# Kernel tuning notes

Hardware: AMD Instinct MI355X
Metric: run time of the kernel (lower is better)

The kernel has to match this reference:

```python
import jax, jax.numpy as jnp
import numpy as np

D = 768
H = 12
HD = 64
S = 77
FF = 3072
EPS = 1e-5


def _layernorm(x, w, b):
    mu = jnp.mean(x, axis=-1, keepdims=True)
    var = jnp.mean(jnp.square(x - mu), axis=-1, keepdims=True)
    return (x - mu) * jax.lax.rsqrt(var + EPS) * w + b


def setup_inputs() -> dict:
    key = jax.random.key(0)
    ks = jax.random.split(key, 18)
    s = 1.0 / np.sqrt(D)
    sf = 1.0 / np.sqrt(FF)
    return {
        "x": jax.random.normal(ks[0], (512, S, D), dtype=jnp.float32),
        "ln1_w": jnp.ones((D,), jnp.float32),
        "ln1_b": jnp.zeros((D,), jnp.float32),
        "qw": jax.random.uniform(ks[1], (D, D), jnp.float32, -s, s),
        "qb": jax.random.uniform(ks[2], (D,), jnp.float32, -s, s),
        "kw": jax.random.uniform(ks[3], (D, D), jnp.float32, -s, s),
        "kb": jax.random.uniform(ks[4], (D,), jnp.float32, -s, s),
        "vw": jax.random.uniform(ks[5], (D, D), jnp.float32, -s, s),
        "vb": jax.random.uniform(ks[6], (D,), jnp.float32, -s, s),
        "ow": jax.random.uniform(ks[7], (D, D), jnp.float32, -s, s),
        "ob": jax.random.uniform(ks[8], (D,), jnp.float32, -s, s),
        "ln2_w": jnp.ones((D,), jnp.float32),
        "ln2_b": jnp.zeros((D,), jnp.float32),
        "fc1_w": jax.random.uniform(ks[9], (FF, D), jnp.float32, -s, s),
        "fc1_b": jax.random.uniform(ks[10], (FF,), jnp.float32, -s, s),
        "fc2_w": jax.random.uniform(ks[11], (D, FF), jnp.float32, -sf, sf),
        "fc2_b": jax.random.uniform(ks[12], (D,), jnp.float32, -sf, sf),
    }


def reference(x, ln1_w, ln1_b, qw, qb, kw, kb, vw, vb, ow, ob,
              ln2_w, ln2_b, fc1_w, fc1_b, fc2_w, fc2_b):
    B = x.shape[0]
    # --- attention block ---
    h = _layernorm(x, ln1_w, ln1_b)
    q = (h @ qw.T + qb) * 0.125
    k = h @ kw.T + kb
    v = h @ vw.T + vb
    # [B, S, H, HD] -> [B, H, S, HD]
    q = q.reshape(B, S, H, HD).transpose(0, 2, 1, 3)
    k = k.reshape(B, S, H, HD).transpose(0, 2, 1, 3)
    v = v.reshape(B, S, H, HD).transpose(0, 2, 1, 3)
    scores = jnp.einsum('bhqd,bhkd->bhqk', q, k)  # [B,H,S,S]
    # causal additive mask: -inf strictly above diagonal
    mask = jnp.triu(jnp.full((S, S), -jnp.inf, dtype=scores.dtype), 1)
    scores = scores + mask
    attn = jax.nn.softmax(scores, axis=-1)
    ctx = jnp.einsum('bhqk,bhkd->bhqd', attn, v)  # [B,H,S,HD]
    ctx = ctx.transpose(0, 2, 1, 3).reshape(B, S, D)
    x = x + (ctx @ ow.T + ob)
    # --- MLP block with QuickGELU ---
    res = x
    h2 = _layernorm(x, ln2_w, ln2_b) @ fc1_w.T + fc1_b
    h2 = h2 * jax.nn.sigmoid(h2 * 1.702)
    return res + (h2 @ fc2_w.T + fc2_b)
```

## Files before the change

### kernel.cpp

```cpp
#include <hip/hip_runtime.h>

typedef unsigned short u16;
typedef __bf16 v8bf __attribute__((ext_vector_type(8)));
typedef unsigned short u16x8 __attribute__((ext_vector_type(8)));
typedef float v4f __attribute__((ext_vector_type(4)));

#define DEV __device__ __forceinline__

constexpr int M_TOK = 512 * 77;

DEV u16 f2bf(float f) {
  union { float f; unsigned int u; } v; v.f = f;
  unsigned int r = v.u + 0x7fffu + ((v.u >> 16) & 1u);
  return (u16)(r >> 16);
}

DEV void gload16(const void* g, void* l) {
  __builtin_amdgcn_global_load_lds((const __attribute__((address_space(1))) void*)g,
                                   (__attribute__((address_space(3))) void*)l, 16, 0, 0);
}

DEV v4f MF(v8bf a, v8bf b, v4f c) {
  return __builtin_amdgcn_mfma_f32_16x16x32_bf16(a, b, c, 0, 0, 0);
}

__global__ void cvt4_k(const float* __restrict__ src, u16* __restrict__ dst, int n4, float scale) {
  int i = blockIdx.x * blockDim.x + threadIdx.x;
  if (i >= n4) return;
  const float4 v = ((const float4*)src)[i];
  ushort4 o;
  o.x = f2bf(v.x * scale); o.y = f2bf(v.y * scale);
  o.z = f2bf(v.z * scale); o.w = f2bf(v.w * scale);
  ((ushort4*)dst)[i] = o;
}

__global__ void qkvb_k(const float* __restrict__ qb, const float* __restrict__ kb,
                       const float* __restrict__ vb, float* __restrict__ dst) {
  int i = blockIdx.x * 256 + threadIdx.x;
  if (i >= 2304) return;
  dst[i] = (i < 768) ? qb[i] * 0.125f : (i < 1536 ? kb[i - 768] : vb[i - 1536]);
}

__global__ __launch_bounds__(256) void ln_k(const float* __restrict__ x, const float* __restrict__ w,
                                            const float* __restrict__ bvec, u16* __restrict__ out, int nrows) {
  const int lane = threadIdx.x & 63;
  const int row = blockIdx.x * 4 + (threadIdx.x >> 6);
  if (row >= nrows) return;
  const float4* xr = (const float4*)(x + (size_t)row * 768);
  float4 v[3];
  float sum = 0.f, sq = 0.f;
#pragma unroll
  for (int t = 0; t < 3; ++t) {
    v[t] = xr[lane + 64 * t];
    sum += v[t].x + v[t].y + v[t].z + v[t].w;
    sq  += v[t].x * v[t].x + v[t].y * v[t].y + v[t].z * v[t].z + v[t].w * v[t].w;
  }
#pragma unroll
  for (int o = 1; o < 64; o <<= 1) { sum += __shfl_xor(sum, o, 64); sq += __shfl_xor(sq, o, 64); }
  const float mean = sum * (1.f / 768.f);
  const float inv = rsqrtf(sq * (1.f / 768.f) - mean * mean + 1e-5f);
  u16* orow = out + (size_t)row * 768;
#pragma unroll
  for (int t = 0; t < 3; ++t) {
    const int c = 4 * (lane + 64 * t);
    ushort4 o4;
    o4.x = f2bf((v[t].x - mean) * inv * w[c + 0] + bvec[c + 0]);
    o4.y = f2bf((v[t].y - mean) * inv * w[c + 1] + bvec[c + 1]);
    o4.z = f2bf((v[t].z - mean) * inv * w[c + 2] + bvec[c + 2]);
    o4.w = f2bf((v[t].w - mean) * inv * w[c + 3] + bvec[c + 3]);
    *(ushort4*)(orow + c) = o4;
  }
}

template <int OUTF32, int ACT, int RES>
__global__ __launch_bounds__(512, 4) void gemm128_k(
    const u16* __restrict__ A, const u16* __restrict__ Bw,
    const float* __restrict__ bias, const float* __restrict__ res,
    void* __restrict__ out, int M, int N, int K, int nbx) {
  __shared__ u16 lds[32768];
  const int tid = threadIdx.x;
  const int lane = tid & 63;
  const int wv = tid >> 6;
  const int wr = wv >> 2, wc = wv & 3;

  const int nwg = gridDim.x;
  const int q8 = nwg >> 3, r8 = nwg & 7;
  const int xcd = blockIdx.x & 7, cidx = blockIdx.x >> 3;
  const int wg = (xcd < r8 ? xcd * (q8 + 1) : r8 * (q8 + 1) + (xcd - r8) * q8) + cidx;
  const int m0 = (wg / nbx) * 128;
  const int n0 = (wg % nbx) * 128;

  const int frow = lane & 15, fq = lane >> 4;
  const int e = frow & 7;
  const int aB0 = (wr * 64 + frow) * 64 + ((fq ^ e) * 8);
  const int bB0 = 8192 + (wc * 32 + frow) * 64 + ((fq ^ e) * 8);

  const int srow = tid >> 3;
  const int cOff = ((tid & 7) ^ (srow & 7)) * 8;
  const u16* pA = A + (size_t)(m0 + srow) * K + cOff;
  const u16* pB = Bw + (size_t)(n0 + srow) * K + cOff;
  const size_t hk = (size_t)K * 64;
  const int ldsW = wv * 512;

#define LD(IDX) (*(const v8bf*)&lds[IDX])
#define BAR() asm volatile("s_barrier" ::: "memory")
#define VM4() asm volatile("s_waitcnt vmcnt(4)" ::: "memory")
#define VM0() asm volatile("s_waitcnt vmcnt(0)" ::: "memory")
#define STA(kt) do { gload16(pA + (size_t)(kt) * 64, &lds[(((kt) & 1) << 14) + ldsW]); \
                     gload16(pA + hk + (size_t)(kt) * 64, &lds[(((kt) & 1) << 14) + 4096 + ldsW]); } while (0)
#define STB(kt) do { gload16(pB + (size_t)(kt) * 64, &lds[(((kt) & 1) << 14) + 8192 + ldsW]); \
                     gload16(pB + hk + (size_t)(kt) * 64, &lds[(((kt) & 1) << 14) + 12288 + ldsW]); } while (0)

  v4f acc[4][2];
#pragma unroll
  for (int i = 0; i < 4; ++i)
#pragma unroll
    for (int j = 0; j < 2; ++j) acc[i][j] = (v4f){0.f, 0.f, 0.f, 0.f};

  const int NT = K >> 6;

  STA(0); STB(0);
  STA(1); STB(1);
  VM4(); BAR();

#define ITER(kt, STG, VM)                                                       \
  do {                                                                          \
    const int sb = ((kt) & 1) << 14;                                            \
    v8bf a0 = LD(sb + aB0), a1 = LD(sb + aB0 + 1024);                           \
    v8bf a2 = LD(sb + aB0 + 2048), a3 = LD(sb + aB0 + 3072);                    \
    v8bf b0 = LD(sb + bB0), b1 = LD(sb + bB0 + 1024);                           \
    v8bf a4 = LD(sb + (aB0 ^ 32)), a5 = LD(sb + (aB0 ^ 32) + 1024);             \
    v8bf a6 = LD(sb + (aB0 ^ 32) + 2048), a7 = LD(sb + (aB0 ^ 32) + 3072);      \
    v8bf b2 = LD(sb + (bB0 ^ 32)), b3 = LD(sb + (bB0 ^ 32) + 1024);             \
    asm volatile("s_waitcnt lgkmcnt(0)" ::: "memory");                          \
    BAR();             \
    if (STG) { STA((kt) + 2); STB((kt) + 2); }                                  \
    if ((VM) == 4) VM4(); else if ((VM) == 0) VM0();                            \
    __builtin_amdgcn_s_setprio(1);                                              \
    acc[0][0] = MF(a0, b0, acc[0][0]); acc[0][1] = MF(a0, b1, acc[0][1]);       \
    acc[1][0] = MF(a1, b0, acc[1][0]); acc[1][1] = MF(a1, b1, acc[1][1]);       \
    acc[2][0] = MF(a2, b0, acc[2][0]); acc[2][1] = MF(a2, b1, acc[2][1]);       \
    acc[3][0] = MF(a3, b0, acc[3][0]); acc[3][1] = MF(a3, b1, acc[3][1]);       \
    acc[0][0] = MF(a4, b2, acc[0][0]); acc[0][1] = MF(a4, b3, acc[0][1]);       \
    acc[1][0] = MF(a5, b2, acc[1][0]); acc[1][1] = MF(a5, b3, acc[1][1]);       \
    acc[2][0] = MF(a6, b2, acc[2][0]); acc[2][1] = MF(a6, b3, acc[2][1]);       \
    acc[3][0] = MF(a7, b2, acc[3][0]); acc[3][1] = MF(a7, b3, acc[3][1]);       \
    __builtin_amdgcn_s_setprio(0);                                              \
    BAR();              \
  } while (0)

  for (int kt = 0; kt < NT - 2; ++kt) ITER(kt, 1, 4);
  ITER(NT - 2, 0, 0);
  ITER(NT - 1, 0, -1);
#undef ITER
#undef LD
#undef BAR
#undef VM4
#undef VM0
#undef STA
#undef STB

#pragma unroll
  for (int i = 0; i < 4; ++i) {
    const int rowb = m0 + wr * 64 + i * 16 + fq * 4;
#pragma unroll
    for (int j = 0; j < 2; ++j) {
      const int col = n0 + wc * 32 + j * 16 + frow;
      const float bv = bias[col];
#pragma unroll
      for (int rr = 0; rr < 4; ++rr) {
        float v = acc[i][j][rr] + bv;
        if (ACT) v = v * (1.f / (1.f + __expf(-1.702f * v)));
        const size_t off = (size_t)(rowb + rr) * N + col;
        if (RES) v += res[off];
        if (OUTF32) ((float*)out)[off] = v;
        else ((u16*)out)[off] = f2bf(v);
      }
    }
  }
}

__global__ __launch_bounds__(256) void attn_k(const u16* __restrict__ qkv, u16* __restrict__ ctx) {
  __shared__ u16 sQK[10240];
  __shared__ u16 sVt[64 * 120];
  __shared__ float sS[80][81];
  const int tid = threadIdx.x;
  const int lane = tid & 63;
  const int wv = tid >> 6;
  const int b = blockIdx.x / 12;
  const int h = blockIdx.x % 12;
  u16* sQ = sQK;
  u16* sK = sQK + 5120;
  u16* sP = sQK;

  for (int i = tid; i < 10240 + 64 * 120; i += 256) {
    if (i < 10240) sQK[i] = 0; else sVt[i - 10240] = 0;
  }
  __syncthreads();

  const size_t tokBase = (size_t)(b * 77) * 2304 + h * 64;
  for (int c = tid; c < 77 * 8; c += 256) {
    const int row = c >> 3, k8 = (c & 7) * 8;
    const size_t src = tokBase + (size_t)row * 2304 + k8;
    *(u16x8*)&sQ[row * 64 + k8] = *(const u16x8*)&qkv[src];
    *(u16x8*)&sK[row * 64 + k8] = *(const u16x8*)&qkv[src + 768];
    u16x8 v = *(const u16x8*)&qkv[src + 1536];
#pragma unroll
    for (int j = 0; j < 8; ++j) sVt[(k8 + j) * 120 + row] = v[j];
  }
  __syncthreads();

  const int frow = lane & 15, fk = (lane >> 4) * 8;
  for (int t = wv; t < 25; t += 4) {
    const int it = t / 5, jt = t % 5;
    v4f acc = {0.f, 0.f, 0.f, 0.f};
#pragma unroll
    for (int kk = 0; kk < 2; ++kk) {
      v8bf a = *(const v8bf*)&sQ[(it * 16 + frow) * 64 + kk * 32 + fk];
      v8bf bb = *(const v8bf*)&sK[(jt * 16 + frow) * 64 + kk * 32 + fk];
      acc = MF(a, bb, acc);
    }
    const int col = jt * 16 + frow;
#pragma unroll
    for (int r = 0; r < 4; ++r) {
      const int row = it * 16 + (lane >> 4) * 4 + r;
      sS[row][col] = (col > row) ? -1e30f : acc[r];
    }
  }
  __syncthreads();

  if (tid < 80) {
    const int row = tid;
    float mx = -1e30f;
    for (int c2 = 0; c2 < 80; ++c2) mx = fmaxf(mx, sS[row][c2]);
    float sum = 0.f;
    for (int c2 = 0; c2 < 80; ++c2) { float e = __expf(sS[row][c2] - mx); sum += e; sS[row][c2] = e; }
    const float inv = 1.f / sum;
    for (int c2 = 0; c2 < 80; ++c2) sP[row * 96 + c2] = f2bf(sS[row][c2] * inv);
    for (int c2 = 80; c2 < 96; ++c2) sP[row * 96 + c2] = 0;
  }
  __syncthreads();

  const size_t outBase = (size_t)(b * 77) * 768 + h * 64;
  for (int t = wv; t < 20; t += 4) {
    const int it = t / 4, jt = t % 4;
    v4f acc = {0.f, 0.f, 0.f, 0.f};
#pragma unroll
    for (int kk = 0; kk < 3; ++kk) {
      v8bf a = *(const v8bf*)&sP[(it * 16 + frow) * 96 + kk * 32 + fk];
      v8bf bb = *(const v8bf*)&sVt[(jt * 16 + frow) * 120 + kk * 32 + fk];
      acc = MF(a, bb, acc);
    }
    const int col = jt * 16 + frow;
#pragma unroll
    for (int r = 0; r < 4; ++r) {
      const int row = it * 16 + (lane >> 4) * 4 + r;
      if (row < 77) ctx[outBase + (size_t)row * 768 + col] = f2bf(acc[r]);
    }
  }
}

extern "C" void kernel_launch(void* const* d_in, const int* in_sizes, int n_in,
                              void* d_out, int out_size, void* d_ws, size_t ws_size,
                              hipStream_t stream) {
  const float* x    = (const float*)d_in[0];
  const float* ln1w = (const float*)d_in[1];
  const float* ln1b = (const float*)d_in[2];
  const float* qw   = (const float*)d_in[3];
  const float* qb   = (const float*)d_in[4];
  const float* kw   = (const float*)d_in[5];
  const float* kb   = (const float*)d_in[6];
  const float* vw   = (const float*)d_in[7];
  const float* vb   = (const float*)d_in[8];
  const float* ow   = (const float*)d_in[9];
  const float* ob   = (const float*)d_in[10];
  const float* ln2w = (const float*)d_in[11];
  const float* ln2b = (const float*)d_in[12];
  const float* f1wf = (const float*)d_in[13];
  const float* f1b  = (const float*)d_in[14];
  const float* f2wf = (const float*)d_in[15];
  const float* f2b  = (const float*)d_in[16];
  float* outp = (float*)d_out;

  char* p = (char*)d_ws;
  auto alloc = [&](size_t bytes) { char* r = p; p += (bytes + 255) & ~(size_t)255; return r; };
  u16* wqkv = (u16*)alloc((size_t)2304 * 768 * 2);
  u16* owb  = (u16*)alloc((size_t)768 * 768 * 2);
  u16* f1w  = (u16*)alloc((size_t)3072 * 768 * 2);
  u16* f2w  = (u16*)alloc((size_t)768 * 3072 * 2);
  float* qkvb = (float*)alloc(2304 * 4);
  u16* bufA = (u16*)alloc((size_t)M_TOK * 768 * 2);
  u16* bufB = (u16*)alloc((size_t)M_TOK * 3072 * 2);

  cvt4_k<<<576, 256, 0, stream>>>(qw, wqkv, 147456, 0.125f);
  cvt4_k<<<576, 256, 0, stream>>>(kw, wqkv + 589824, 147456, 1.f);
  cvt4_k<<<576, 256, 0, stream>>>(vw, wqkv + 1179648, 147456, 1.f);
  cvt4_k<<<576, 256, 0, stream>>>(ow, owb, 147456, 1.f);
  cvt4_k<<<2304, 256, 0, stream>>>(f1wf, f1w, 589824, 1.f);
  cvt4_k<<<2304, 256, 0, stream>>>(f2wf, f2w, 589824, 1.f);
  qkvb_k<<<9, 256, 0, stream>>>(qb, kb, vb, qkvb);

  ln_k<<<M_TOK / 4, 256, 0, stream>>>(x, ln1w, ln1b, bufA, M_TOK);
  gemm128_k<0, 0, 0><<<308 * 18, 512, 0, stream>>>(bufA, wqkv, qkvb, nullptr, bufB, M_TOK, 2304, 768, 18);
  attn_k<<<512 * 12, 256, 0, stream>>>(bufB, bufA);
  gemm128_k<1, 0, 1><<<308 * 6, 512, 0, stream>>>(bufA, owb, ob, x, outp, M_TOK, 768, 768, 6);
  ln_k<<<M_TOK / 4, 256, 0, stream>>>(outp, ln2w, ln2b, bufA, M_TOK);
  gemm128_k<0, 1, 0><<<308 * 24, 512, 0, stream>>>(bufA, f1w, f1b, nullptr, bufB, M_TOK, 3072, 768, 24);
  gemm128_k<1, 0, 1><<<308 * 6, 512, 0, stream>>>(bufB, f2w, f2b, outp, outp, M_TOK, 768, 3072, 6);
}
```

Before: 952.3 us.

## Use 4-wave GEMM blocks with 64x64 per-wave tiles instead of 8 waves

The 128x128 GEMM tile moves from 8 waves (each 64x32) to 4 waves (each 64x64), with 256 threads per block. Each thread now issues four global-to-LDS loads per operand per k-step, and the wait count rises to match. The goal is more MFMA work per LDS fragment read and fewer waves to synchronise. The cost is twice the accumulator registers per wave and fewer waves available to hide latency.

```diff
diff --git a/kernel.cpp b/kernel.cpp
--- a/kernel.cpp
+++ b/kernel.cpp
@@ -73,7 +73,7 @@
 }
 
 template <int OUTF32, int ACT, int RES>
-__global__ __launch_bounds__(512, 4) void gemm128_k(
+__global__ __launch_bounds__(256, 2) void gemm128_k(
     const u16* __restrict__ A, const u16* __restrict__ Bw,
     const float* __restrict__ bias, const float* __restrict__ res,
     void* __restrict__ out, int M, int N, int K, int nbx) {
@@ -81,7 +81,7 @@
   const int tid = threadIdx.x;
   const int lane = tid & 63;
   const int wv = tid >> 6;
-  const int wr = wv >> 2, wc = wv & 3;
+  const int wr = wv >> 1, wc = wv & 1;
 
   const int nwg = gridDim.x;
   const int q8 = nwg >> 3, r8 = nwg & 7;
@@ -93,69 +93,85 @@
   const int frow = lane & 15, fq = lane >> 4;
   const int e = frow & 7;
   const int aB0 = (wr * 64 + frow) * 64 + ((fq ^ e) * 8);
-  const int bB0 = 8192 + (wc * 32 + frow) * 64 + ((fq ^ e) * 8);
+  const int bB0 = 8192 + (wc * 64 + frow) * 64 + ((fq ^ e) * 8);
 
   const int srow = tid >> 3;
   const int cOff = ((tid & 7) ^ (srow & 7)) * 8;
   const u16* pA = A + (size_t)(m0 + srow) * K + cOff;
   const u16* pB = Bw + (size_t)(n0 + srow) * K + cOff;
-  const size_t hk = (size_t)K * 64;
+  const size_t K32 = (size_t)K * 32;
   const int ldsW = wv * 512;
 
 #define LD(IDX) (*(const v8bf*)&lds[IDX])
 #define BAR() asm volatile("s_barrier" ::: "memory")
-#define VM4() asm volatile("s_waitcnt vmcnt(4)" ::: "memory")
+#define VM8() asm volatile("s_waitcnt vmcnt(8)" ::: "memory")
 #define VM0() asm volatile("s_waitcnt vmcnt(0)" ::: "memory")
-#define STA(kt) do { gload16(pA + (size_t)(kt) * 64, &lds[(((kt) & 1) << 14) + ldsW]); \
-                     gload16(pA + hk + (size_t)(kt) * 64, &lds[(((kt) & 1) << 14) + 4096 + ldsW]); } while (0)
-#define STB(kt) do { gload16(pB + (size_t)(kt) * 64, &lds[(((kt) & 1) << 14) + 8192 + ldsW]); \
-                     gload16(pB + hk + (size_t)(kt) * 64, &lds[(((kt) & 1) << 14) + 12288 + ldsW]); } while (0)
-
-  v4f acc[4][2];
+#define STA(kt) do { const int sb_ = ((kt) & 1) << 14;                              \
+    gload16(pA + 0 * K32 + (size_t)(kt) * 64, &lds[sb_ + 0 * 2048 + ldsW]);         \
+    gload16(pA + 1 * K32 + (size_t)(kt) * 64, &lds[sb_ + 1 * 2048 + ldsW]);         \
+    gload16(pA + 2 * K32 + (size_t)(kt) * 64, &lds[sb_ + 2 * 2048 + ldsW]);         \
+    gload16(pA + 3 * K32 + (size_t)(kt) * 64, &lds[sb_ + 3 * 2048 + ldsW]); } while (0)
+#define STB(kt) do { const int sb_ = (((kt) & 1) << 14) + 8192;                     \
+    gload16(pB + 0 * K32 + (size_t)(kt) * 64, &lds[sb_ + 0 * 2048 + ldsW]);         \
+    gload16(pB + 1 * K32 + (size_t)(kt) * 64, &lds[sb_ + 1 * 2048 + ldsW]);         \
+    gload16(pB + 2 * K32 + (size_t)(kt) * 64, &lds[sb_ + 2 * 2048 + ldsW]);         \
+    gload16(pB + 3 * K32 + (size_t)(kt) * 64, &lds[sb_ + 3 * 2048 + ldsW]); } while (0)
+
+  v4f acc[4][4];
 #pragma unroll
   for (int i = 0; i < 4; ++i)
 #pragma unroll
-    for (int j = 0; j < 2; ++j) acc[i][j] = (v4f){0.f, 0.f, 0.f, 0.f};
+    for (int j = 0; j < 4; ++j) acc[i][j] = (v4f){0.f, 0.f, 0.f, 0.f};
 
   const int NT = K >> 6;
 
   STA(0); STB(0);
   STA(1); STB(1);
-  VM4(); BAR();
+  VM8(); BAR();
 
 #define ITER(kt, STG, VM)                                                       \
   do {                                                                          \
     const int sb = ((kt) & 1) << 14;                                            \
     v8bf a0 = LD(sb + aB0), a1 = LD(sb + aB0 + 1024);                           \
     v8bf a2 = LD(sb + aB0 + 2048), a3 = LD(sb + aB0 + 3072);                    \
-    v8bf b0 = LD(sb + bB0), b1 = LD(sb + bB0 + 1024);                           \
     v8bf a4 = LD(sb + (aB0 ^ 32)), a5 = LD(sb + (aB0 ^ 32) + 1024);             \
     v8bf a6 = LD(sb + (aB0 ^ 32) + 2048), a7 = LD(sb + (aB0 ^ 32) + 3072);      \
-    v8bf b2 = LD(sb + (bB0 ^ 32)), b3 = LD(sb + (bB0 ^ 32) + 1024);             \
+    v8bf b0 = LD(sb + bB0), b1 = LD(sb + bB0 + 1024);                           \
+    v8bf b2 = LD(sb + bB0 + 2048), b3 = LD(sb + bB0 + 3072);                    \
+    v8bf b4 = LD(sb + (bB0 ^ 32)), b5 = LD(sb + (bB0 ^ 32) + 1024);             \
+    v8bf b6 = LD(sb + (bB0 ^ 32) + 2048), b7 = LD(sb + (bB0 ^ 32) + 3072);      \
     asm volatile("s_waitcnt lgkmcnt(0)" ::: "memory");                          \
     BAR();             \
     if (STG) { STA((kt) + 2); STB((kt) + 2); }                                  \
-    if ((VM) == 4) VM4(); else if ((VM) == 0) VM0();                            \
+    if ((VM) == 8) VM8(); else if ((VM) == 0) VM0();                            \
     __builtin_amdgcn_s_setprio(1);                                              \
     acc[0][0] = MF(a0, b0, acc[0][0]); acc[0][1] = MF(a0, b1, acc[0][1]);       \
+    acc[0][2] = MF(a0, b2, acc[0][2]); acc[0][3] = MF(a0, b3, acc[0][3]);       \
     acc[1][0] = MF(a1, b0, acc[1][0]); acc[1][1] = MF(a1, b1, acc[1][1]);       \
+    acc[1][2] = MF(a1, b2, acc[1][2]); acc[1][3] = MF(a1, b3, acc[1][3]);       \
     acc[2][0] = MF(a2, b0, acc[2][0]); acc[2][1] = MF(a2, b1, acc[2][1]);       \
+    acc[2][2] = MF(a2, b2, acc[2][2]); acc[2][3] = MF(a2, b3, acc[2][3]);       \
     acc[3][0] = MF(a3, b0, acc[3][0]); acc[3][1] = MF(a3, b1, acc[3][1]);       \
-    acc[0][0] = MF(a4, b2, acc[0][0]); acc[0][1] = MF(a4, b3, acc[0][1]);       \
-    acc[1][0] = MF(a5, b2, acc[1][0]); acc[1][1] = MF(a5, b3, acc[1][1]);       \
-    acc[2][0] = MF(a6, b2, acc[2][0]); acc[2][1] = MF(a6, b3, acc[2][1]);       \
-    acc[3][0] = MF(a7, b2, acc[3][0]); acc[3][1] = MF(a7, b3, acc[3][1]);       \
+    acc[3][2] = MF(a3, b2, acc[3][2]); acc[3][3] = MF(a3, b3, acc[3][3]);       \
+    acc[0][0] = MF(a4, b4, acc[0][0]); acc[0][1] = MF(a4, b5, acc[0][1]);       \
+    acc[0][2] = MF(a4, b6, acc[0][2]); acc[0][3] = MF(a4, b7, acc[0][3]);       \
+    acc[1][0] = MF(a5, b4, acc[1][0]); acc[1][1] = MF(a5, b5, acc[1][1]);       \
+    acc[1][2] = MF(a5, b6, acc[1][2]); acc[1][3] = MF(a5, b7, acc[1][3]);       \
+    acc[2][0] = MF(a6, b4, acc[2][0]); acc[2][1] = MF(a6, b5, acc[2][1]);       \
+    acc[2][2] = MF(a6, b6, acc[2][2]); acc[2][3] = MF(a6, b7, acc[2][3]);       \
+    acc[3][0] = MF(a7, b4, acc[3][0]); acc[3][1] = MF(a7, b5, acc[3][1]);       \
+    acc[3][2] = MF(a7, b6, acc[3][2]); acc[3][3] = MF(a7, b7, acc[3][3]);       \
     __builtin_amdgcn_s_setprio(0);                                              \
     BAR();              \
   } while (0)
 
-  for (int kt = 0; kt < NT - 2; ++kt) ITER(kt, 1, 4);
+  for (int kt = 0; kt < NT - 2; ++kt) ITER(kt, 1, 8);
   ITER(NT - 2, 0, 0);
   ITER(NT - 1, 0, -1);
 #undef ITER
 #undef LD
 #undef BAR
-#undef VM4
+#undef VM8
 #undef VM0
 #undef STA
 #undef STB
@@ -164,8 +180,8 @@
   for (int i = 0; i < 4; ++i) {
     const int rowb = m0 + wr * 64 + i * 16 + fq * 4;
 #pragma unroll
-    for (int j = 0; j < 2; ++j) {
-      const int col = n0 + wc * 32 + j * 16 + frow;
+    for (int j = 0; j < 4; ++j) {
+      const int col = n0 + wc * 64 + j * 16 + frow;
       const float bv = bias[col];
 #pragma unroll
       for (int rr = 0; rr < 4; ++rr) {
@@ -301,10 +317,10 @@
   qkvb_k<<<9, 256, 0, stream>>>(qb, kb, vb, qkvb);
 
   ln_k<<<M_TOK / 4, 256, 0, stream>>>(x, ln1w, ln1b, bufA, M_TOK);
-  gemm128_k<0, 0, 0><<<308 * 18, 512, 0, stream>>>(bufA, wqkv, qkvb, nullptr, bufB, M_TOK, 2304, 768, 18);
+  gemm128_k<0, 0, 0><<<308 * 18, 256, 0, stream>>>(bufA, wqkv, qkvb, nullptr, bufB, M_TOK, 2304, 768, 18);
   attn_k<<<512 * 12, 256, 0, stream>>>(bufB, bufA);
-  gemm128_k<1, 0, 1><<<308 * 6, 512, 0, stream>>>(bufA, owb, ob, x, outp, M_TOK, 768, 768, 6);
+  gemm128_k<1, 0, 1><<<308 * 6, 256, 0, stream>>>(bufA, owb, ob, x, outp, M_TOK, 768, 768, 6);
   ln_k<<<M_TOK / 4, 256, 0, stream>>>(outp, ln2w, ln2b, bufA, M_TOK);
-  gemm128_k<0, 1, 0><<<308 * 24, 512, 0, stream>>>(bufA, f1w, f1b, nullptr, bufB, M_TOK, 3072, 768, 24);
-  gemm128_k<1, 0, 1><<<308 * 6, 512, 0, stream>>>(bufB, f2w, f2b, outp, outp, M_TOK, 768, 3072, 6);
-}
+  gemm128_k<0, 1, 0><<<308 * 24, 256, 0, stream>>>(bufA, f1w, f1b, nullptr, bufB, M_TOK, 3072, 768, 24);
+  gemm128_k<1, 0, 1><<<308 * 6, 256, 0, stream>>>(bufB, f2w, f2b, outp, outp, M_TOK, 768, 3072, 6);
+}
```

Result: no change. 940.7 us (-1.2%).

## Widen GEMM tile to 128x256 with triple-buffered LDS and register prefetch

Applied to the files above, without the earlier changes.

The GEMM kernel's N tile doubles to 256, so each wave computes a 64x64 sub-tile with 16 accumulators instead of 8. A three-stage LDS ring replaces the double buffer, and the next k-step's fragments are double-buffered in registers so LDS reads overlap the MFMAs. One barrier per iteration replaces two. The aim is more MFMA work per LDS byte and less exposed load latency, at the cost of more registers and 144KB of LDS, which cuts occupancy to two workgroups per CU and halves the grid.

```diff
diff --git a/kernel.cpp b/kernel.cpp
--- a/kernel.cpp
+++ b/kernel.cpp
@@ -73,11 +73,11 @@
 }
 
 template <int OUTF32, int ACT, int RES>
-__global__ __launch_bounds__(512, 4) void gemm128_k(
+__global__ __launch_bounds__(512, 2) void gemmP_k(
     const u16* __restrict__ A, const u16* __restrict__ Bw,
     const float* __restrict__ bias, const float* __restrict__ res,
     void* __restrict__ out, int M, int N, int K, int nbx) {
-  __shared__ u16 lds[32768];
+  __shared__ u16 lds[73728];
   const int tid = threadIdx.x;
   const int lane = tid & 63;
   const int wv = tid >> 6;
@@ -88,84 +88,99 @@
   const int xcd = blockIdx.x & 7, cidx = blockIdx.x >> 3;
   const int wg = (xcd < r8 ? xcd * (q8 + 1) : r8 * (q8 + 1) + (xcd - r8) * q8) + cidx;
   const int m0 = (wg / nbx) * 128;
-  const int n0 = (wg % nbx) * 128;
+  const int n0 = (wg % nbx) * 256;
 
   const int frow = lane & 15, fq = lane >> 4;
   const int e = frow & 7;
-  const int aB0 = (wr * 64 + frow) * 64 + ((fq ^ e) * 8);
-  const int bB0 = 8192 + (wc * 32 + frow) * 64 + ((fq ^ e) * 8);
+  const int aB = (wr * 64 + frow) * 64 + ((fq ^ e) * 8);
+  const int bB = 8192 + (wc * 64 + frow) * 64 + ((fq ^ e) * 8);
 
   const int srow = tid >> 3;
   const int cOff = ((tid & 7) ^ (srow & 7)) * 8;
   const u16* pA = A + (size_t)(m0 + srow) * K + cOff;
   const u16* pB = Bw + (size_t)(n0 + srow) * K + cOff;
-  const size_t hk = (size_t)K * 64;
+  const size_t K64 = (size_t)K * 64;
   const int ldsW = wv * 512;
 
 #define LD(IDX) (*(const v8bf*)&lds[IDX])
 #define BAR() asm volatile("s_barrier" ::: "memory")
-#define VM4() asm volatile("s_waitcnt vmcnt(4)" ::: "memory")
-#define VM0() asm volatile("s_waitcnt vmcnt(0)" ::: "memory")
-#define STA(kt) do { gload16(pA + (size_t)(kt) * 64, &lds[(((kt) & 1) << 14) + ldsW]); \
-                     gload16(pA + hk + (size_t)(kt) * 64, &lds[(((kt) & 1) << 14) + 4096 + ldsW]); } while (0)
-#define STB(kt) do { gload16(pB + (size_t)(kt) * 64, &lds[(((kt) & 1) << 14) + 8192 + ldsW]); \
-                     gload16(pB + hk + (size_t)(kt) * 64, &lds[(((kt) & 1) << 14) + 12288 + ldsW]); } while (0)
-
-  v4f acc[4][2];
+#define STAGE(t, s) do {                                                        \
+    const int sb_ = (s) * 24576;                                                \
+    gload16(pA + 0 * K64 + (size_t)(t) * 64, &lds[sb_ + 0 * 4096 + ldsW]);      \
+    gload16(pA + 1 * K64 + (size_t)(t) * 64, &lds[sb_ + 1 * 4096 + ldsW]);      \
+    gload16(pB + 0 * K64 + (size_t)(t) * 64, &lds[sb_ + 8192 + 0 * 4096 + ldsW]); \
+    gload16(pB + 1 * K64 + (size_t)(t) * 64, &lds[sb_ + 8192 + 1 * 4096 + ldsW]); \
+    gload16(pB + 2 * K64 + (size_t)(t) * 64, &lds[sb_ + 8192 + 2 * 4096 + ldsW]); \
+    gload16(pB + 3 * K64 + (size_t)(t) * 64, &lds[sb_ + 8192 + 3 * 4096 + ldsW]); \
+  } while (0)
+#define READSET(S, rb) do {                                                     \
+    _Pragma("unroll")                                                           \
+    for (int i_ = 0; i_ < 4; ++i_) {                                            \
+      Af[S][i_]     = LD((rb) + aB + i_ * 1024);                                \
+      Af[S][4 + i_] = LD(((rb) + aB + i_ * 1024) ^ 32);                         \
+      Bf[S][i_]     = LD((rb) + bB + i_ * 1024);                                \
+      Bf[S][4 + i_] = LD(((rb) + bB + i_ * 1024) ^ 32);                         \
+    }                                                                           \
+  } while (0)
+#define MFMA32(S) do {                                                          \
+    _Pragma("unroll")                                                           \
+    for (int i_ = 0; i_ < 4; ++i_)                                              \
+      _Pragma("unroll")                                                         \
+      for (int j_ = 0; j_ < 4; ++j_)                                            \
+        acc[i_][j_] = MF(Af[S][i_], Bf[S][j_], acc[i_][j_]);                    \
+    _Pragma("unroll")                                                           \
+    for (int i_ = 0; i_ < 4; ++i_)                                              \
+      _Pragma("unroll")                                                         \
+      for (int j_ = 0; j_ < 4; ++j_)                                            \
+        acc[i_][j_] = MF(Af[S][4 + i_], Bf[S][4 + j_], acc[i_][j_]);            \
+  } while (0)
+#define BODY(kt, S, NS) do {                                                    \
+    const int stg_ = (kt) + 3;                                                  \
+    if (stg_ < NT) STAGE(stg_, stg_ % 3);                                       \
+    if ((kt) + 1 < NT) { READSET(NS, (((kt) + 1) % 3) * 24576); }               \
+    __builtin_amdgcn_s_setprio(1);                                              \
+    MFMA32(S);                                                                  \
+    __builtin_amdgcn_s_setprio(0);                                              \
+    asm volatile("s_waitcnt lgkmcnt(0)" ::: "memory");                          \
+    __builtin_amdgcn_sched_barrier(0);                                          \
+    if (stg_ < NT) { asm volatile("s_waitcnt vmcnt(6)" ::: "memory"); }         \
+    else           { asm volatile("s_waitcnt vmcnt(0)" ::: "memory"); }         \
+    __builtin_amdgcn_sched_barrier(0);                                          \
+    BAR();                                                                      \
+  } while (0)
+
+  v8bf Af[2][8], Bf[2][8];
+  v4f acc[4][4];
 #pragma unroll
   for (int i = 0; i < 4; ++i)
 #pragma unroll
-    for (int j = 0; j < 2; ++j) acc[i][j] = (v4f){0.f, 0.f, 0.f, 0.f};
+    for (int j = 0; j < 4; ++j) acc[i][j] = (v4f){0.f, 0.f, 0.f, 0.f};
 
   const int NT = K >> 6;
 
-  STA(0); STB(0);
-  STA(1); STB(1);
-  VM4(); BAR();
-
-#define ITER(kt, STG, VM)                                                       \
-  do {                                                                          \
-    const int sb = ((kt) & 1) << 14;                                            \
-    v8bf a0 = LD(sb + aB0), a1 = LD(sb + aB0 + 1024);                           \
-    v8bf a2 = LD(sb + aB0 + 2048), a3 = LD(sb + aB0 + 3072);                    \
-    v8bf b0 = LD(sb + bB0), b1 = LD(sb + bB0 + 1024);                           \
-    v8bf a4 = LD(sb + (aB0 ^ 32)), a5 = LD(sb + (aB0 ^ 32) + 1024);             \
-    v8bf a6 = LD(sb + (aB0 ^ 32) + 2048), a7 = LD(sb + (aB0 ^ 32) + 3072);      \
-    v8bf b2 = LD(sb + (bB0 ^ 32)), b3 = LD(sb + (bB0 ^ 32) + 1024);             \
-    asm volatile("s_waitcnt lgkmcnt(0)" ::: "memory");                          \
-    BAR();             \
-    if (STG) { STA((kt) + 2); STB((kt) + 2); }                                  \
-    if ((VM) == 4) VM4(); else if ((VM) == 0) VM0();                            \
-    __builtin_amdgcn_s_setprio(1);                                              \
-    acc[0][0] = MF(a0, b0, acc[0][0]); acc[0][1] = MF(a0, b1, acc[0][1]);       \
-    acc[1][0] = MF(a1, b0, acc[1][0]); acc[1][1] = MF(a1, b1, acc[1][1]);       \
-    acc[2][0] = MF(a2, b0, acc[2][0]); acc[2][1] = MF(a2, b1, acc[2][1]);       \
-    acc[3][0] = MF(a3, b0, acc[3][0]); acc[3][1] = MF(a3, b1, acc[3][1]);       \
-    acc[0][0] = MF(a4, b2, acc[0][0]); acc[0][1] = MF(a4, b3, acc[0][1]);       \
-    acc[1][0] = MF(a5, b2, acc[1][0]); acc[1][1] = MF(a5, b3, acc[1][1]);       \
-    acc[2][0] = MF(a6, b2, acc[2][0]); acc[2][1] = MF(a6, b3, acc[2][1]);       \
-    acc[3][0] = MF(a7, b2, acc[3][0]); acc[3][1] = MF(a7, b3, acc[3][1]);       \
-    __builtin_amdgcn_s_setprio(0);                                              \
-    BAR();              \
-  } while (0)
-
-  for (int kt = 0; kt < NT - 2; ++kt) ITER(kt, 1, 4);
-  ITER(NT - 2, 0, 0);
-  ITER(NT - 1, 0, -1);
-#undef ITER
+  STAGE(0, 0); STAGE(1, 1); STAGE(2, 2);
+  asm volatile("s_waitcnt vmcnt(6)" ::: "memory");
+  BAR();
+  READSET(0, 0);
+
+  for (int kt2 = 0; kt2 < (NT >> 1); ++kt2) {
+    const int kt = kt2 * 2;
+    BODY(kt, 0, 1);
+    BODY(kt + 1, 1, 0);
+  }
+#undef BODY
+#undef MFMA32
+#undef READSET
+#undef STAGE
 #undef LD
 #undef BAR
-#undef VM4
-#undef VM0
-#undef STA
-#undef STB
 
 #pragma unroll
   for (int i = 0; i < 4; ++i) {
     const int rowb = m0 + wr * 64 + i * 16 + fq * 4;
 #pragma unroll
-    for (int j = 0; j < 2; ++j) {
-      const int col = n0 + wc * 32 + j * 16 + frow;
+    for (int j = 0; j < 4; ++j) {
+      const int col = n0 + wc * 64 + j * 16 + frow;
       const float bv = bias[col];
 #pragma unroll
       for (int rr = 0; rr < 4; ++rr) {
@@ -301,10 +316,10 @@
   qkvb_k<<<9, 256, 0, stream>>>(qb, kb, vb, qkvb);
 
   ln_k<<<M_TOK / 4, 256, 0, stream>>>(x, ln1w, ln1b, bufA, M_TOK);
-  gemm128_k<0, 0, 0><<<308 * 18, 512, 0, stream>>>(bufA, wqkv, qkvb, nullptr, bufB, M_TOK, 2304, 768, 18);
+  gemmP_k<0, 0, 0><<<308 * 9, 512, 0, stream>>>(bufA, wqkv, qkvb, nullptr, bufB, M_TOK, 2304, 768, 9);
   attn_k<<<512 * 12, 256, 0, stream>>>(bufB, bufA);
-  gemm128_k<1, 0, 1><<<308 * 6, 512, 0, stream>>>(bufA, owb, ob, x, outp, M_TOK, 768, 768, 6);
+  gemmP_k<1, 0, 1><<<308 * 3, 512, 0, stream>>>(bufA, owb, ob, x, outp, M_TOK, 768, 768, 3);
   ln_k<<<M_TOK / 4, 256, 0, stream>>>(outp, ln2w, ln2b, bufA, M_TOK);
-  gemm128_k<0, 1, 0><<<308 * 24, 512, 0, stream>>>(bufA, f1w, f1b, nullptr, bufB, M_TOK, 3072, 768, 24);
-  gemm128_k<1, 0, 1><<<308 * 6, 512, 0, stream>>>(bufB, f2w, f2b, outp, outp, M_TOK, 768, 3072, 6);
-}
+  gemmP_k<0, 1, 0><<<308 * 12, 512, 0, stream>>>(bufA, f1w, f1b, nullptr, bufB, M_TOK, 3072, 768, 12);
+  gemmP_k<1, 0, 1><<<308 * 3, 512, 0, stream>>>(bufB, f2w, f2b, outp, outp, M_TOK, 768, 3072, 3);
+}
```

Result: slower. 1.034 ms (+8.6%).
